# Optimization experiments

Measured on AMD Instinct MI355X. Metric: run time of the kernel, lower is better.

Reference implementation:

```python
import jax, jax.numpy as jnp
import numpy as np

C_TOTAL, C_SEL = 64, 32
IN_F, OUT_F = 128, 128
BATCH = 16384


def setup_inputs() -> dict:
    key = jax.random.key(0)
    k1, k2, k3, k4 = jax.random.split(key, 4)
    inp = jax.random.normal(k1, (BATCH, C_SEL, IN_F), dtype=jnp.float32)
    # kaiming-uniform-ish scale for weight, small bias per reset_parameters
    bound_w = 1.0 / np.sqrt(IN_F)
    weight = jax.random.uniform(k2, (C_TOTAL, OUT_F, IN_F), dtype=jnp.float32,
                                minval=-bound_w, maxval=bound_w) * np.sqrt(3.0)
    bias = jax.random.uniform(k3, (C_TOTAL, OUT_F), dtype=jnp.float32,
                              minval=-bound_w, maxval=bound_w)
    channels = jax.random.randint(k4, (C_SEL,), 0, C_TOTAL, dtype=jnp.int32)
    return {"input": inp, "weight": weight, "bias": bias, "channels": channels}


def reference(input, weight, bias, channels):
    # Gather per-channel weights/biases, then batched linear over the channel dim.
    # Original torch: (W * input[..., None, :]).sum(-1) + B with W broadcast to
    # (1, C_sel, out, in) -- mathematically a per-channel matmul.
    W = weight[channels]          # (C_sel, out, in)
    B = bias[channels]            # (C_sel, out)
    out = jnp.einsum('bci,coi->bco', input, W)  # (batch, C_sel, out)
    return out + B[None, :, :]
```

## Files before the change

### kernel.cpp

```cpp
#include <hip/hip_runtime.h>
#include <hip/hip_bf16.h>

#define BATCH   16384
#define C_SEL   32
#define C_TOTAL 64
#define IN_F    128
#define OUT_F   128

#define BM      128

typedef __bf16 bf16x8 __attribute__((ext_vector_type(8)));
typedef float  f32x4  __attribute__((ext_vector_type(4)));

__global__ __launch_bounds__(256) void pl_mfma_kernel(
    const float* __restrict__ inp,
    const float* __restrict__ weight,
    const float* __restrict__ bias,
    const int*   __restrict__ channels,
    float*       __restrict__ out)
{
    __shared__ __bf16 ldsW[OUT_F * IN_F];

    const int gx = blockIdx.x;
    const int c  = gx & 31;
    const int m0 = (gx >> 5) * BM;

    const int ch = channels[c];

    const int t  = threadIdx.x;
    const int w  = t >> 6;
    const int l  = t & 63;
    const int lr = l & 15;
    const int lg = l >> 4;

    bf16x8 afrag[2][4];
    #pragma unroll
    for (int mt = 0; mt < 2; ++mt) {
        const size_t m = (size_t)(m0 + w * 32 + mt * 16 + lr);
        const float* arow = inp + (m * C_SEL + (size_t)c) * IN_F;
        #pragma unroll
        for (int ks = 0; ks < 4; ++ks) {
            const float* p = arow + ks * 32 + lg * 8;
            const float4 f0 = *reinterpret_cast<const float4*>(p);
            const float4 f1 = *reinterpret_cast<const float4*>(p + 4);
            bf16x8 a;
            a[0] = (__bf16)f0.x; a[1] = (__bf16)f0.y; a[2] = (__bf16)f0.z; a[3] = (__bf16)f0.w;
            a[4] = (__bf16)f1.x; a[5] = (__bf16)f1.y; a[6] = (__bf16)f1.z; a[7] = (__bf16)f1.w;
            afrag[mt][ks] = a;
        }
    }

    const float* wsrc = weight + (size_t)ch * (OUT_F * IN_F);
    #pragma unroll
    for (int i = 0; i < 8; ++i) {
        const int fidx = i * 2048 + t * 8;
        const int row  = fidx >> 7;
        const int u    = (fidx & 127) >> 3;
        const float4 f0 = *reinterpret_cast<const float4*>(wsrc + fidx);
        const float4 f1 = *reinterpret_cast<const float4*>(wsrc + fidx + 4);
        bf16x8 v;
        v[0] = (__bf16)f0.x; v[1] = (__bf16)f0.y; v[2] = (__bf16)f0.z; v[3] = (__bf16)f0.w;
        v[4] = (__bf16)f1.x; v[5] = (__bf16)f1.y; v[6] = (__bf16)f1.z; v[7] = (__bf16)f1.w;
        const int up = u ^ (row & 7);
        *reinterpret_cast<bf16x8*>(&ldsW[row * IN_F + up * 8]) = v;
    }
    __syncthreads();

    f32x4 acc[2][8];
    #pragma unroll
    for (int mt = 0; mt < 2; ++mt)
        #pragma unroll
        for (int nt = 0; nt < 8; ++nt) {
            f32x4 z = {0.f, 0.f, 0.f, 0.f};
            acc[mt][nt] = z;
        }

    #pragma unroll
    for (int ks = 0; ks < 4; ++ks) {
        #pragma unroll
        for (int nt = 0; nt < 8; ++nt) {
            const int row = nt * 16 + lr;
            const int u   = (ks * 4 + lg) ^ (lr & 7);
            const bf16x8 b = *reinterpret_cast<const bf16x8*>(
                &ldsW[row * IN_F + u * 8]);
            acc[0][nt] = __builtin_amdgcn_mfma_f32_16x16x32_bf16(afrag[0][ks], b, acc[0][nt], 0, 0, 0);
            acc[1][nt] = __builtin_amdgcn_mfma_f32_16x16x32_bf16(afrag[1][ks], b, acc[1][nt], 0, 0, 0);
        }
    }

    const float* brow = bias + (size_t)ch * OUT_F;
    #pragma unroll
    for (int mt = 0; mt < 2; ++mt) {
        #pragma unroll
        for (int j = 0; j < 4; ++j) {
            const size_t m = (size_t)(m0 + w * 32 + mt * 16 + lg * 4 + j);
            float* orow = out + (m * C_SEL + (size_t)c) * OUT_F;
            #pragma unroll
            for (int nt = 0; nt < 8; ++nt) {
                orow[nt * 16 + lr] = acc[mt][nt][j] + brow[nt * 16 + lr];
            }
        }
    }
}

extern "C" void kernel_launch(void* const* d_in, const int* in_sizes, int n_in,
                              void* d_out, int out_size, void* d_ws, size_t ws_size,
                              hipStream_t stream) {
    const float* inp      = (const float*)d_in[0];
    const float* weight   = (const float*)d_in[1];
    const float* bias     = (const float*)d_in[2];
    const int*   channels = (const int*)d_in[3];
    float*       out      = (float*)d_out;

    dim3 grid(C_SEL * (BATCH / BM));
    dim3 block(256);
    pl_mfma_kernel<<<grid, block, 0, stream>>>(inp, weight, bias, channels, out);
}
```

Baseline: 142.1 us.

## Make blocks persistent over batch tiles with register-prefetched input and nontemporal stores

The grid shrinks to 32 channels x 32 groups, and each block loops over 8 batch tiles of 64 rows. It converts and stages the channel weight into LDS once and reuses it across all tiles. The next tile's input rows are prefetched into registers while the current tile's MFMAs run, bias is hoisted into registers, and outputs use nontemporal stores. This amortises the per-block weight load and conversion and overlaps global loads with compute. In exchange it gives fewer blocks (1024) and a serialized loop per block.

After: 210.4 us. +48.1%, slower.

```diff
diff --git a/kernel.cpp b/kernel.cpp
--- a/kernel.cpp
+++ b/kernel.cpp
@@ -7,12 +7,21 @@
 #define IN_F    128
 #define OUT_F   128
 
-#define BM      128
+#define BM      64
+#define NGRP    32
+#define NJOBS   8
 
 typedef __bf16 bf16x8 __attribute__((ext_vector_type(8)));
 typedef float  f32x4  __attribute__((ext_vector_type(4)));
 
-__global__ __launch_bounds__(256) void pl_mfma_kernel(
+__device__ __forceinline__ bf16x8 cvt_bf16x8(const float4 f0, const float4 f1) {
+    bf16x8 a;
+    a[0] = (__bf16)f0.x; a[1] = (__bf16)f0.y; a[2] = (__bf16)f0.z; a[3] = (__bf16)f0.w;
+    a[4] = (__bf16)f1.x; a[5] = (__bf16)f1.y; a[6] = (__bf16)f1.z; a[7] = (__bf16)f1.w;
+    return a;
+}
+
+__global__ __launch_bounds__(256, 4) void pl_mfma_kernel(
     const float* __restrict__ inp,
     const float* __restrict__ weight,
     const float* __restrict__ bias,
@@ -21,11 +30,10 @@
 {
     __shared__ __bf16 ldsW[OUT_F * IN_F];
 
-    const int gx = blockIdx.x;
-    const int c  = gx & 31;
-    const int m0 = (gx >> 5) * BM;
-
-    const int ch = channels[c];
+    const int bid = blockIdx.x;
+    const int c   = bid & 31;
+    const int g   = bid >> 5;
+    const int ch  = channels[c];
 
     const int t  = threadIdx.x;
     const int w  = t >> 6;
@@ -33,20 +41,15 @@
     const int lr = l & 15;
     const int lg = l >> 4;
 
-    bf16x8 afrag[2][4];
-    #pragma unroll
-    for (int mt = 0; mt < 2; ++mt) {
-        const size_t m = (size_t)(m0 + w * 32 + mt * 16 + lr);
+    float4 ra[8];
+    {
+        const size_t m = (size_t)g * BM + w * 16 + lr;
         const float* arow = inp + (m * C_SEL + (size_t)c) * IN_F;
         #pragma unroll
         for (int ks = 0; ks < 4; ++ks) {
             const float* p = arow + ks * 32 + lg * 8;
-            const float4 f0 = *reinterpret_cast<const float4*>(p);
-            const float4 f1 = *reinterpret_cast<const float4*>(p + 4);
-            bf16x8 a;
-            a[0] = (__bf16)f0.x; a[1] = (__bf16)f0.y; a[2] = (__bf16)f0.z; a[3] = (__bf16)f0.w;
-            a[4] = (__bf16)f1.x; a[5] = (__bf16)f1.y; a[6] = (__bf16)f1.z; a[7] = (__bf16)f1.w;
-            afrag[mt][ks] = a;
+            ra[ks * 2]     = *reinterpret_cast<const float4*>(p);
+            ra[ks * 2 + 1] = *reinterpret_cast<const float4*>(p + 4);
         }
     }
 
@@ -58,46 +61,56 @@
         const int u    = (fidx & 127) >> 3;
         const float4 f0 = *reinterpret_cast<const float4*>(wsrc + fidx);
         const float4 f1 = *reinterpret_cast<const float4*>(wsrc + fidx + 4);
-        bf16x8 v;
-        v[0] = (__bf16)f0.x; v[1] = (__bf16)f0.y; v[2] = (__bf16)f0.z; v[3] = (__bf16)f0.w;
-        v[4] = (__bf16)f1.x; v[5] = (__bf16)f1.y; v[6] = (__bf16)f1.z; v[7] = (__bf16)f1.w;
         const int up = u ^ (row & 7);
-        *reinterpret_cast<bf16x8*>(&ldsW[row * IN_F + up * 8]) = v;
+        *reinterpret_cast<bf16x8*>(&ldsW[row * IN_F + up * 8]) = cvt_bf16x8(f0, f1);
     }
+
+    float bv[8];
+    const float* brow = bias + (size_t)ch * OUT_F;
+    #pragma unroll
+    for (int nt = 0; nt < 8; ++nt) bv[nt] = brow[nt * 16 + lr];
+
     __syncthreads();
 
-    f32x4 acc[2][8];
-    #pragma unroll
-    for (int mt = 0; mt < 2; ++mt)
+    for (int j = 0; j < NJOBS; ++j) {
+        bf16x8 af[4];
         #pragma unroll
-        for (int nt = 0; nt < 8; ++nt) {
-            f32x4 z = {0.f, 0.f, 0.f, 0.f};
-            acc[mt][nt] = z;
+        for (int ks = 0; ks < 4; ++ks) af[ks] = cvt_bf16x8(ra[ks * 2], ra[ks * 2 + 1]);
+
+        if (j + 1 < NJOBS) {
+            const size_t mn = ((size_t)(j + 1) * NGRP + g) * BM + w * 16 + lr;
+            const float* arow = inp + (mn * C_SEL + (size_t)c) * IN_F;
+            #pragma unroll
+            for (int ks = 0; ks < 4; ++ks) {
+                const float* p = arow + ks * 32 + lg * 8;
+                ra[ks * 2]     = *reinterpret_cast<const float4*>(p);
+                ra[ks * 2 + 1] = *reinterpret_cast<const float4*>(p + 4);
+            }
         }
 
-    #pragma unroll
-    for (int ks = 0; ks < 4; ++ks) {
+        f32x4 acc[8];
         #pragma unroll
-        for (int nt = 0; nt < 8; ++nt) {
-            const int row = nt * 16 + lr;
-            const int u   = (ks * 4 + lg) ^ (lr & 7);
-            const bf16x8 b = *reinterpret_cast<const bf16x8*>(
-                &ldsW[row * IN_F + u * 8]);
-            acc[0][nt] = __builtin_amdgcn_mfma_f32_16x16x32_bf16(afrag[0][ks], b, acc[0][nt], 0, 0, 0);
-            acc[1][nt] = __builtin_amdgcn_mfma_f32_16x16x32_bf16(afrag[1][ks], b, acc[1][nt], 0, 0, 0);
+        for (int nt = 0; nt < 8; ++nt) { f32x4 z = {0.f,0.f,0.f,0.f}; acc[nt] = z; }
+
+        #pragma unroll
+        for (int ks = 0; ks < 4; ++ks) {
+            #pragma unroll
+            for (int nt = 0; nt < 8; ++nt) {
+                const int row = nt * 16 + lr;
+                const int u   = (ks * 4 + lg) ^ (lr & 7);
+                const bf16x8 b = *reinterpret_cast<const bf16x8*>(&ldsW[row * IN_F + u * 8]);
+                acc[nt] = __builtin_amdgcn_mfma_f32_16x16x32_bf16(af[ks], b, acc[nt], 0, 0, 0);
+            }
         }
-    }
 
-    const float* brow = bias + (size_t)ch * OUT_F;
-    #pragma unroll
-    for (int mt = 0; mt < 2; ++mt) {
+        const size_t mtile = ((size_t)j * NGRP + g) * BM;
         #pragma unroll
-        for (int j = 0; j < 4; ++j) {
-            const size_t m = (size_t)(m0 + w * 32 + mt * 16 + lg * 4 + j);
+        for (int j2 = 0; j2 < 4; ++j2) {
+            const size_t m = mtile + w * 16 + lg * 4 + j2;
             float* orow = out + (m * C_SEL + (size_t)c) * OUT_F;
             #pragma unroll
             for (int nt = 0; nt < 8; ++nt) {
-                orow[nt * 16 + lr] = acc[mt][nt][j] + brow[nt * 16 + lr];
+                __builtin_nontemporal_store(acc[nt][j2] + bv[nt], &orow[nt * 16 + lr]);
             }
         }
     }
@@ -112,7 +125,7 @@
     const int*   channels = (const int*)d_in[3];
     float*       out      = (float*)d_out;
 
-    dim3 grid(C_SEL * (BATCH / BM));
+    dim3 grid(C_SEL * NGRP);
     dim3 block(256);
     pl_mfma_kernel<<<grid, block, 0, stream>>>(inp, weight, bias, channels, out);
 }
```
